# Performance work log

Measured on AMD Instinct MI355X. Metric: run time of the kernel, lower is better.

## Reference

```python
import jax, jax.numpy as jnp
import numpy as np

N_SHIFT = 23          # self.n in the torch module
OUTPUT_BIT = 8
INT31_MAX = 2147483647.0  # 2**31 - 1


def floor_ste(x):
    # straight-through floor: forward floor, backward identity
    return x + jax.lax.stop_gradient(jnp.floor(x) - x)


def int_exp_shift(x_int, scaling_factor):
    # integer-only exp approximation via shift decomposition
    x_int = x_int + floor_ste(x_int / 2.0) - floor_ste(x_int / 16.0)  # x*(1+1/2-1/16) ~ x*ln2^-1 trick
    x0_int = jax.lax.stop_gradient(jnp.floor(-1.0 / scaling_factor))   # -ln2 in integer domain (no grad)
    x_int = jnp.maximum(x_int, N_SHIFT * x0_int)
    q = floor_ste(x_int / x0_int)                 # integer quotient, in [0, N_SHIFT]
    r = x_int - x0_int * q                        # remainder
    exp_int = r / 2.0 - x0_int
    exp_int = jnp.maximum(floor_ste(exp_int * jnp.exp2(N_SHIFT - q)), 0.0)
    return exp_int


def setup_inputs() -> dict:
    key = jax.random.key(0)
    k1, _ = jax.random.split(key)
    x = jax.random.normal(k1, (64, 197, 3072), dtype=jnp.float32)
    # realistic per-tensor activation quantization scale
    scaling_factor = jnp.ones((1,), dtype=jnp.float32) * 0.02
    return {"x": x, "scaling_factor": scaling_factor}


def reference(x, scaling_factor):
    pre_x_int = x / scaling_factor                      # [B, T, H] integer-domain input
    sf_sig = scaling_factor * 1.702                     # sigmoid(1.702*x) GELU approx scale
    x_int_max = jnp.max(pre_x_int, axis=-1, keepdims=True)   # [B, T, 1]
    x_int = pre_x_int - x_int_max                       # shift for numerical range
    exp_int = int_exp_shift(x_int, sf_sig)              # exp(x - m)
    exp_int_max = int_exp_shift(-x_int_max, sf_sig)     # exp(-m) == exp(0 - m)
    exp_int_sum = jnp.minimum(exp_int + exp_int_max, INT31_MAX)
    factor = floor_ste(INT31_MAX / exp_int_sum)
    sigmoid_int = floor_ste(exp_int * factor / 2.0 ** (31 - OUTPUT_BIT + 1))
    out_sf = scaling_factor * (1.0 / 2.0 ** (OUTPUT_BIT - 1))
    x_int_out = pre_x_int * sigmoid_int
    return x_int_out * out_sf, out_sf
```

## Files before the change

kernel.cpp:

```cpp
#include <hip/hip_runtime.h>
#include <math.h>


#define ROWLEN   3072
#define NTHREADS 256
#define VPT      12

typedef float f32x4 __attribute__((ext_vector_type(4)));

__device__ __forceinline__ float crdiv(float a, float b, float y) {
    #pragma clang fp contract(off)
    float q0 = a * y;
    float r  = fmaf(-q0, b, a);
    return fmaf(r, y, q0);
}

__device__ __forceinline__ float int_exp_fast(float xi, float x0, float y_x0,
                                              float c23x0) {
    #pragma clang fp contract(off)
    float t = (xi + floorf(xi * 0.5f)) - floorf(xi * 0.0625f);
    t = fmaxf(t, c23x0);
    float q = floorf(t * y_x0);
    float r = t - x0 * q;
    float e = r * 0.5f - x0;
    e = floorf(ldexpf(e, 23 - (int)q));
    return fmaxf(e, 0.0f);
}

__device__ __forceinline__ float int_exp_cr(float xi, float x0, float y_x0,
                                            float c23x0) {
    #pragma clang fp contract(off)
    float t = (xi + floorf(xi * 0.5f)) - floorf(xi * 0.0625f);
    t = fmaxf(t, c23x0);
    float q = floorf(crdiv(t, x0, y_x0));
    float r = t - x0 * q;
    float e = r * 0.5f - x0;
    e = floorf(ldexpf(e, 23 - (int)q));
    return fmaxf(e, 0.0f);
}

__global__ __launch_bounds__(NTHREADS)
void intgelu_kernel(const float* __restrict__ x, const float* __restrict__ sfp,
                    float* __restrict__ out, long long scalar_idx) {
    #pragma clang fp contract(off)
    const int tid  = threadIdx.x;
    const int lane = tid & 63;
    const int row  = blockIdx.x * (NTHREADS / 64) + (tid >> 6);

    const float sf     = sfp[0];
    const float y_sf   = 1.0f / sf;
    const float x0     = floorf(-1.0f / (sf * 1.702f));
    const float y_x0   = 1.0f / x0;
    const float c23x0  = 23.0f * x0;
    const float out_sf = sf * 0.0078125f;

    const f32x4* xr = reinterpret_cast<const f32x4*>(x + (size_t)row * ROWLEN);

    f32x4 v[VPT];
    #pragma unroll
    for (int c = 0; c < VPT; ++c)
        v[c] = xr[c * 64 + lane];

    float lmax = -INFINITY;
    #pragma unroll
    for (int c = 0; c < VPT; ++c)
        lmax = fmaxf(lmax, fmaxf(fmaxf(v[c][0], v[c][1]), fmaxf(v[c][2], v[c][3])));

    #pragma unroll
    for (int off = 32; off > 0; off >>= 1)
        lmax = fmaxf(lmax, __shfl_xor(lmax, off, 64));

    #pragma unroll
    for (int c = 0; c < VPT; ++c) {
        v[c][0] = crdiv(v[c][0], sf, y_sf);
        v[c][1] = crdiv(v[c][1], sf, y_sf);
        v[c][2] = crdiv(v[c][2], sf, y_sf);
        v[c][3] = crdiv(v[c][3], sf, y_sf);
    }
    const float m  = crdiv(lmax, sf, y_sf);
    const float em = int_exp_cr(0.0f - m, x0, y_x0, c23x0);

    f32x4* outr = reinterpret_cast<f32x4*>(out + (size_t)row * ROWLEN);
    #pragma unroll
    for (int c = 0; c < VPT; ++c) {
        f32x4 o;
        #pragma unroll
        for (int j = 0; j < 4; ++j) {
            float pp = v[c][j];
            float e  = int_exp_fast(pp - m, x0, y_x0, c23x0);
            float s  = e + em;
            float f  = floorf(2147483648.0f / s);
            float sg = floorf((e * f) * 5.9604644775390625e-8f);
            o[j] = (pp * sg) * out_sf;
        }
        outr[c * 64 + lane] = o;
    }

    if (row == 0 && lane == 0) out[scalar_idx] = out_sf;
}

extern "C" void kernel_launch(void* const* d_in, const int* in_sizes, int n_in,
                              void* d_out, int out_size, void* d_ws, size_t ws_size,
                              hipStream_t stream) {
    const float* x   = (const float*)d_in[0];
    const float* sfp = (const float*)d_in[1];
    float*       out = (float*)d_out;
    const int nrows  = in_sizes[0] / ROWLEN;
    const long long scalar_idx = (long long)out_size - 1;
    const int grid = nrows / (NTHREADS / 64);
    intgelu_kernel<<<grid, NTHREADS, 0, stream>>>(x, sfp, out, scalar_idx);
}
```

Baseline: 270.8 us.

## Process four rows per wave with double-buffered register prefetch

```diff
diff --git a/kernel.cpp b/kernel.cpp
--- a/kernel.cpp
+++ b/kernel.cpp
@@ -4,6 +4,7 @@
 
 #define ROWLEN   3072
 #define NTHREADS 256
+#define WPB      (NTHREADS / 64)
 #define VPT      12
 
 typedef float f32x4 __attribute__((ext_vector_type(4)));
@@ -39,44 +40,28 @@
     return fmaxf(e, 0.0f);
 }
 
-__global__ __launch_bounds__(NTHREADS)
-void intgelu_kernel(const float* __restrict__ x, const float* __restrict__ sfp,
-                    float* __restrict__ out, long long scalar_idx) {
+__device__ __forceinline__ void load_row(f32x4* __restrict__ v,
+                                         const float* __restrict__ x,
+                                         int row, int lane) {
+    const f32x4* xr = reinterpret_cast<const f32x4*>(x + (size_t)row * ROWLEN);
+    #pragma unroll
+    for (int c = 0; c < VPT; ++c) v[c] = xr[c * 64 + lane];
+}
+
+__device__ __forceinline__ void process_row(const f32x4* __restrict__ v,
+                                            float* __restrict__ out, int row,
+                                            int lane, float sf, float y_sf,
+                                            float x0, float y_x0, float c23x0,
+                                            float out_sf) {
     #pragma clang fp contract(off)
-    const int tid  = threadIdx.x;
-    const int lane = tid & 63;
-    const int row  = blockIdx.x * (NTHREADS / 64) + (tid >> 6);
-
-    const float sf     = sfp[0];
-    const float y_sf   = 1.0f / sf;
-    const float x0     = floorf(-1.0f / (sf * 1.702f));
-    const float y_x0   = 1.0f / x0;
-    const float c23x0  = 23.0f * x0;
-    const float out_sf = sf * 0.0078125f;
-
-    const f32x4* xr = reinterpret_cast<const f32x4*>(x + (size_t)row * ROWLEN);
-
-    f32x4 v[VPT];
-    #pragma unroll
-    for (int c = 0; c < VPT; ++c)
-        v[c] = xr[c * 64 + lane];
-
     float lmax = -INFINITY;
     #pragma unroll
     for (int c = 0; c < VPT; ++c)
         lmax = fmaxf(lmax, fmaxf(fmaxf(v[c][0], v[c][1]), fmaxf(v[c][2], v[c][3])));
-
     #pragma unroll
     for (int off = 32; off > 0; off >>= 1)
         lmax = fmaxf(lmax, __shfl_xor(lmax, off, 64));
 
-    #pragma unroll
-    for (int c = 0; c < VPT; ++c) {
-        v[c][0] = crdiv(v[c][0], sf, y_sf);
-        v[c][1] = crdiv(v[c][1], sf, y_sf);
-        v[c][2] = crdiv(v[c][2], sf, y_sf);
-        v[c][3] = crdiv(v[c][3], sf, y_sf);
-    }
     const float m  = crdiv(lmax, sf, y_sf);
     const float em = int_exp_cr(0.0f - m, x0, y_x0, c23x0);
 
@@ -86,7 +71,7 @@
         f32x4 o;
         #pragma unroll
         for (int j = 0; j < 4; ++j) {
-            float pp = v[c][j];
+            float pp = crdiv(v[c][j], sf, y_sf);
             float e  = int_exp_fast(pp - m, x0, y_x0, c23x0);
             float s  = e + em;
             float f  = floorf(2147483648.0f / s);
@@ -95,8 +80,37 @@
         }
         outr[c * 64 + lane] = o;
     }
+}
 
-    if (row == 0 && lane == 0) out[scalar_idx] = out_sf;
+__global__ __launch_bounds__(NTHREADS)
+void intgelu_kernel(const float* __restrict__ x, const float* __restrict__ sfp,
+                    float* __restrict__ out, int nrows, long long scalar_idx) {
+    #pragma clang fp contract(off)
+    const int lane = threadIdx.x & 63;
+    const int wid  = blockIdx.x * WPB + (threadIdx.x >> 6);
+    const int S    = gridDim.x * WPB;
+
+    const float sf     = sfp[0];
+    const float y_sf   = 1.0f / sf;
+    const float x0     = floorf(-1.0f / (sf * 1.702f));
+    const float y_x0   = 1.0f / x0;
+    const float c23x0  = 23.0f * x0;
+    const float out_sf = sf * 0.0078125f;
+
+    if (wid == 0 && lane == 0) out[scalar_idx] = out_sf;
+
+    const int r0 = wid, r1 = wid + S, r2 = wid + 2 * S, r3 = wid + 3 * S;
+    if (r0 >= nrows) return;
+
+    f32x4 A[VPT], B[VPT];
+    load_row(A, x, r0, lane);
+    if (r1 < nrows) load_row(B, x, r1, lane);
+    process_row(A, out, r0, lane, sf, y_sf, x0, y_x0, c23x0, out_sf);
+    if (r2 < nrows) load_row(A, x, r2, lane);
+    if (r1 < nrows) process_row(B, out, r1, lane, sf, y_sf, x0, y_x0, c23x0, out_sf);
+    if (r3 < nrows) load_row(B, x, r3, lane);
+    if (r2 < nrows) process_row(A, out, r2, lane, sf, y_sf, x0, y_x0, c23x0, out_sf);
+    if (r3 < nrows) process_row(B, out, r3, lane, sf, y_sf, x0, y_x0, c23x0, out_sf);
 }
 
 extern "C" void kernel_launch(void* const* d_in, const int* in_sizes, int n_in,
@@ -107,6 +121,7 @@
     float*       out = (float*)d_out;
     const int nrows  = in_sizes[0] / ROWLEN;
     const long long scalar_idx = (long long)out_size - 1;
-    const int grid = nrows / (NTHREADS / 64);
-    intgelu_kernel<<<grid, NTHREADS, 0, stream>>>(x, sfp, out, scalar_idx);
+    const int nwaves = (nrows + 3) / 4;
+    const int grid   = (nwaves + WPB - 1) / WPB;
+    intgelu_kernel<<<grid, NTHREADS, 0, stream>>>(x, sfp, out, nrows, scalar_idx);
 }
```

After: 287.6 us. +6.2%, slower.
